# Optimization experiments

Hardware: AMD Instinct MI355X
Metric: run time of the kernel (lower is better)

Reference implementation:

```python
import jax, jax.numpy as jnp
import numpy as np

B, S, D = 512, 81, 1024
NH, DH = 16, 64
C, H1, G, FF = 32, 256, 256, 4096


def _ln(x, g, b, eps=1e-5):
    m = x.mean(-1, keepdims=True)
    v = ((x - m) ** 2).mean(-1, keepdims=True)
    return (x - m) * jax.lax.rsqrt(v + eps) * g + b


def _mish(x):
    return x * jnp.tanh(jax.nn.softplus(x))


def setup_inputs() -> dict:
    key = jax.random.key(0)
    ks = iter(jax.random.split(key, 32))
    n = lambda shape, s=0.02: jax.random.normal(next(ks), shape, jnp.float32) * s
    return {
        "x": jax.random.normal(next(ks), (B, S, D), jnp.float32),
        "w_compress": n((D, C)), "b_compress": jnp.zeros((C,)),
        "w_d1": n((S * C, H1)), "b_d1": jnp.zeros((H1,)),
        "ln1s_g": jnp.ones((H1,)), "ln1s_b": jnp.zeros((H1,)),
        "w_d2": n((H1, NH * G)), "b_d2": jnp.zeros((NH * G,)),
        "ln2s_g": jnp.ones((NH * G,)), "ln2s_b": jnp.zeros((NH * G,)),
        "w_gg": n((G, S * S)), "b_gg": jnp.zeros((S * S,)),
        "wq": n((D, D)), "bq": jnp.zeros((D,)),
        "wk": n((D, D)), "bk": jnp.zeros((D,)),
        "wv": n((D, D)), "bv": jnp.zeros((D,)),
        "wo": n((D, D)), "bo": jnp.zeros((D,)),
        "ln1_g": jnp.ones((D,)), "ln1_b": jnp.zeros((D,)),
        "w_f1": n((D, FF)), "b_f1": jnp.zeros((FF,)),
        "w_f2": n((FF, D)), "b_f2": jnp.zeros((D,)),
        "fln_g": jnp.ones((D,)), "fln_b": jnp.zeros((D,)),
    }


def reference(x, w_compress, b_compress, w_d1, b_d1, ln1s_g, ln1s_b,
              w_d2, b_d2, ln2s_g, ln2s_b, w_gg, b_gg,
              wq, bq, wk, bk, wv, bv, wo, bo, ln1_g, ln1_b,
              w_f1, b_f1, w_f2, b_f2, fln_g, fln_b):
    b = x.shape[0]
    # --- Smolgen: per-position attention bias ---
    h = jax.nn.silu(x @ w_compress + b_compress).reshape(b, S * C)
    h = jax.nn.silu(_ln(h @ w_d1 + b_d1, ln1s_g, ln1s_b))
    h = jax.nn.silu(_ln(h @ w_d2 + b_d2, ln2s_g, ln2s_b))
    h = h.reshape(b, NH, G)
    smol_bias = (h @ w_gg + b_gg).reshape(b, NH, S, S)
    # --- Attention with additive bias ---
    q = (x @ wq + bq).reshape(b, S, NH, DH)
    k = (x @ wk + bk).reshape(b, S, NH, DH)
    v = (x @ wv + bv).reshape(b, S, NH, DH)
    scores = jnp.einsum("bqhd,bkhd->bhqk", q, k) / np.sqrt(DH) + smol_bias
    attn = jax.nn.softmax(scores, axis=-1)
    out = jnp.einsum("bhqk,bkhd->bqhd", attn, v).reshape(b, S, D)
    h = _ln(out @ wo + bo + x, ln1_g, ln1_b)
    # --- FFN ---
    f = _mish(h @ w_f1 + b_f1)
    return _ln(f @ w_f2 + b_f2 + h, fln_g, fln_b)
```

## Files before the change

### kernel.cpp

```cpp
#include <hip/hip_runtime.h>
#include <hip/hip_bf16.h>
#include <cstdint>
#include <cstdio>

using bf16 = __hip_bfloat16;
typedef __attribute__((ext_vector_type(8))) short bf16x8;
typedef __attribute__((ext_vector_type(4))) float f32x4;

__device__ __forceinline__ void gload_lds16(const void* g, void* l) {
  __builtin_amdgcn_global_load_lds((__attribute__((address_space(1))) void*)g,
                                   (__attribute__((address_space(3))) void*)l,
                                   16, 0, 0);
}

__device__ __forceinline__ float bfu2f(unsigned short u) {
  return __uint_as_float((unsigned int)u << 16);
}
__device__ __forceinline__ unsigned short f2bfu(float f) {
  bf16 b = __float2bfloat16(f);
  return *(unsigned short*)&b;
}

enum { EP_NONE = 0, EP_SILU = 1, EP_MISH = 2, EP_RES = 3, EP_RESB = 4 };

template<int EPI>
__global__ __launch_bounds__(512, 1)
void gemm256(const bf16* __restrict__ A, const bf16* __restrict__ Bt,
             int N, int Nb, int K, int gx,
             const float* __restrict__ bias,
             const float* __restrict__ residf,
             const bf16* __restrict__ residb,
             bf16* __restrict__ outb)
{
  __shared__ char lds[131072];
  const int tid  = threadIdx.x;
  const int lane = tid & 63;
  const int wid  = tid >> 6;
  const int wm = wid >> 2, wn = wid & 3;
  const int lr = lane & 15, kg = lane >> 4;

  const int nwg = gridDim.x;
  const int q8 = nwg >> 3, r8 = nwg & 7;
  const int xcd = blockIdx.x & 7, idx = blockIdx.x >> 3;
  const int wg2 = (xcd < r8 ? xcd * (q8 + 1) : r8 * (q8 + 1) + (xcd - r8) * q8) + idx;
  const int bx = wg2 % gx, by = wg2 / gx;
  const long brow = (long)bx * 256, bcol = (long)by * 256;

  const size_t rb = (size_t)K * 2;
  const int r0   = wid * 8 + (lane >> 3);
  const int coff = ((lane & 7) ^ (lane >> 3)) << 4;
  const char* aS = (const char*)A  + (size_t)(brow + r0) * rb + coff;
  const char* bS = (const char*)Bt + (size_t)(bcol + r0) * rb + coff;
  char* ldsA = lds;
  char* ldsB = lds + 65536;
  const int luni = wid * 1024;

  const int ktiles = K >> 6;

  auto stage = [&](int t, int cur) {
    const size_t tb = (size_t)t * 128;
#pragma unroll
    for (int q = 0; q < 4; q++) {
      gload_lds16(aS + tb + (size_t)q * 64 * rb, ldsA + cur * 32768 + q * 8192 + luni);
      gload_lds16(bS + tb + (size_t)q * 64 * rb, ldsB + cur * 32768 + q * 8192 + luni);
    }
  };

  f32x4 acc[8][4] = {};

  stage(0, 0);
  stage(1, 1);

  const int swz   = (lr & 7) << 4;
  const int abase = (wm * 128 + lr) * 128;
  const int bbase = (wn * 64 + lr) * 128;

  for (int t = 0; t < ktiles; ++t) {
    const int cur = t & 1;
    if (t + 1 < ktiles) asm volatile("s_waitcnt vmcnt(8)" ::: "memory");
    else                asm volatile("s_waitcnt vmcnt(0)" ::: "memory");
    __builtin_amdgcn_s_barrier();
    const char* pA = ldsA + cur * 32768;
    const char* pB = ldsB + cur * 32768;
#pragma unroll
    for (int ks = 0; ks < 2; ks++) {
      const int kb = ((((ks << 2) + kg) << 4)) ^ swz;
      bf16x8 a[8], b[4];
#pragma unroll
      for (int i = 0; i < 8; i++) a[i] = *(const bf16x8*)(pA + abase + i * 2048 + kb);
#pragma unroll
      for (int j = 0; j < 4; j++) b[j] = *(const bf16x8*)(pB + bbase + j * 2048 + kb);
      __builtin_amdgcn_s_setprio(1);
#pragma unroll
      for (int i = 0; i < 8; i++)
#pragma unroll
        for (int j = 0; j < 4; j++)
          acc[i][j] = __builtin_amdgcn_mfma_f32_16x16x32_bf16(a[i], b[j], acc[i][j], 0, 0, 0);
      __builtin_amdgcn_s_setprio(0);
    }
    __builtin_amdgcn_s_barrier();
    if (t + 2 < ktiles) stage(t + 2, cur);
  }

  char* lC = lds;
  const int cr = kg * 4;
#pragma unroll
  for (int j = 0; j < 4; j++) {
    const int tcol = wn * 64 + j * 16 + lr;
    const long gcol = bcol + tcol;
    const float bv = (gcol < Nb) ? bias[gcol] : 0.f;
#pragma unroll
    for (int i = 0; i < 8; i++) {
#pragma unroll
      for (int r = 0; r < 4; r++) {
        const int row = wm * 128 + i * 16 + cr + r;
        float v = acc[i][j][r] + bv;
        if constexpr (EPI == EP_MISH) {
          float e = __expf(fminf(v, 20.f));
          float u = (1.f + e); u *= u;
          v = v * (u - 1.f) / (u + 1.f);
        }
        *(unsigned short*)(lC + row * 512 + ((tcol * 2) ^ ((row & 12) << 3))) = f2bfu(v);
      }
    }
  }
  __syncthreads();
  const int trow = tid >> 5;
  const int tcb  = (tid & 31) * 16;
#pragma unroll
  for (int it = 0; it < 16; ++it) {
    const int row = it * 16 + trow;
    bf16x8 vv = *(const bf16x8*)(lC + row * 512 + (tcb ^ ((row & 12) << 3)));
    const long grow = brow + row;
    bf16* dst = outb + grow * (long)N + bcol + (tcb >> 1);
    if constexpr (EPI == EP_RES) {
      const float* rs = residf + grow * (long)N + bcol + (tcb >> 1);
      float4 ra = *(const float4*)rs, rb2 = *(const float4*)(rs + 4);
      float rv[8] = {ra.x, ra.y, ra.z, ra.w, rb2.x, rb2.y, rb2.z, rb2.w};
      bf16x8 ov;
#pragma unroll
      for (int e = 0; e < 8; e++)
        ov[e] = (short)f2bfu(bfu2f((unsigned short)vv[e]) + rv[e]);
      *(bf16x8*)dst = ov;
    } else if constexpr (EPI == EP_RESB) {
      bf16x8 rb3 = *(const bf16x8*)(residb + grow * (long)N + bcol + (tcb >> 1));
      bf16x8 ov;
#pragma unroll
      for (int e = 0; e < 8; e++)
        ov[e] = (short)f2bfu(bfu2f((unsigned short)vv[e]) + bfu2f((unsigned short)rb3[e]));
      *(bf16x8*)dst = ov;
    } else {
      *(bf16x8*)dst = vv;
    }
  }
}

template<int EPI, bool OUTF>
__global__ __launch_bounds__(256)
void gemm_kernel(const bf16* __restrict__ A, const bf16* __restrict__ Bt,
                 int M, int N, int K,
                 const float* __restrict__ bias,
                 const float* __restrict__ residf,
                 const bf16* __restrict__ residb,
                 float* __restrict__ outf, bf16* __restrict__ outb)
{
  __shared__ bf16 lA[128 * 32];
  __shared__ bf16 lB[128 * 32];
  const int tid  = threadIdx.x;
  const int lane = tid & 63;
  const int wvid = tid >> 6;
  const int wr = (wvid >> 1) * 64;
  const int wc = (wvid & 1) * 64;
  const long brow = (long)blockIdx.x * 128;
  const long bcol = (long)blockIdx.y * 128;
  const int lr = lane & 15;
  const int k8 = (lane >> 4) * 8;

  const int lofs0 = wvid * 1024;
  const int lofs1 = lofs0 + 4096;
  const int o0 = lofs0 + lane * 16;
  const int o1 = o0 + 4096;
  const int r0 = o0 >> 6, c0 = o0 & 63;
  const int r1 = o1 >> 6, c1 = o1 & 63;

  f32x4 acc[4][4] = {};

  for (int k0 = 0; k0 < K; k0 += 32) {
    const long kb = (long)k0 * 2;
    gload_lds16((const char*)A  + ((brow + r0) * (long)K) * 2 + kb + c0, (char*)lA + lofs0);
    gload_lds16((const char*)A  + ((brow + r1) * (long)K) * 2 + kb + c1, (char*)lA + lofs1);
    gload_lds16((const char*)Bt + ((bcol + r0) * (long)K) * 2 + kb + c0, (char*)lB + lofs0);
    gload_lds16((const char*)Bt + ((bcol + r1) * (long)K) * 2 + kb + c1, (char*)lB + lofs1);
    __syncthreads();
    bf16x8 af[4], bf_[4];
#pragma unroll
    for (int i = 0; i < 4; i++)
      af[i] = *(const bf16x8*)&lA[(wr + i * 16 + lr) * 32 + k8];
#pragma unroll
    for (int j = 0; j < 4; j++)
      bf_[j] = *(const bf16x8*)&lB[(wc + j * 16 + lr) * 32 + k8];
#pragma unroll
    for (int i = 0; i < 4; i++)
#pragma unroll
      for (int j = 0; j < 4; j++)
        acc[i][j] = __builtin_amdgcn_mfma_f32_16x16x32_bf16(af[i], bf_[j], acc[i][j], 0, 0, 0);
    __syncthreads();
  }

  const int cr = (lane >> 4) * 4;
  const int cc = lane & 15;
#pragma unroll
  for (int j = 0; j < 4; j++) {
    const long col = bcol + wc + j * 16 + cc;
    if (col >= N) continue;
    const float bv = bias[col];
#pragma unroll
    for (int i = 0; i < 4; i++) {
#pragma unroll
      for (int r = 0; r < 4; r++) {
        const long row = brow + wr + i * 16 + cr + r;
        float v = acc[i][j][r] + bv;
        if constexpr (EPI == EP_RES)  v += residf[row * N + col];
        if constexpr (EPI == EP_RESB) v += __bfloat162float(residb[row * N + col]);
        if constexpr (EPI == EP_SILU) v = v / (1.f + __expf(-v));
        if constexpr (EPI == EP_MISH) {
          float t = __expf(fminf(v, 20.f));
          float u = (1.f + t); u *= u;
          v = v * (u - 1.f) / (u + 1.f);
        }
        if constexpr (OUTF) outf[row * N + col] = v;
        else                outb[row * N + col] = __float2bfloat16(v);
      }
    }
  }
}

__global__ __launch_bounds__(256)
void transpose_to_bf16(const float* __restrict__ W, bf16* __restrict__ Bt,
                       int K, int N, int Npad)
{
  __shared__ float tile[32][33];
  const int n0 = blockIdx.x * 32, k0 = blockIdx.y * 32;
  const int tx = threadIdx.x, ty = threadIdx.y;
  for (int r = ty; r < 32; r += 8) {
    int k = k0 + r, n = n0 + tx;
    tile[r][tx] = (k < K && n < N) ? W[(size_t)k * N + n] : 0.f;
  }
  __syncthreads();
  for (int r = ty; r < 32; r += 8) {
    int n = n0 + r, k = k0 + tx;
    if (n < Npad && k < K) Bt[(size_t)n * K + k] = __float2bfloat16(tile[tx][r]);
  }
}

__global__ __launch_bounds__(256)
void cvt_f32_bf16(const float* __restrict__ in, bf16* __restrict__ out, long n)
{
  long i = ((long)blockIdx.x * 256 + threadIdx.x) * 4;
  const long stride = (long)gridDim.x * 256 * 4;
  for (; i < n; i += stride) {
    float4 v = *(const float4*)(in + i);
    out[i]     = __float2bfloat16(v.x);
    out[i + 1] = __float2bfloat16(v.y);
    out[i + 2] = __float2bfloat16(v.z);
    out[i + 3] = __float2bfloat16(v.w);
  }
}

__global__ __launch_bounds__(256)
void pack3(const float* __restrict__ a, const float* __restrict__ b,
           const float* __restrict__ c, float* __restrict__ o, int n)
{
  int i = blockIdx.x * 256 + threadIdx.x;
  if (i < n) { o[i] = a[i]; o[n + i] = b[i]; o[2 * n + i] = c[i]; }
}

template<int ACT>
__global__ __launch_bounds__(256)
void ln_rows(const float* __restrict__ inf, const float* __restrict__ g,
             const float* __restrict__ be, bf16* __restrict__ ob, int C)
{
  const long row = blockIdx.x;
  float s = 0.f, ss = 0.f;
  for (int c = threadIdx.x; c < C; c += 256) {
    float v = inf[row * C + c];
    s += v; ss += v * v;
  }
#pragma unroll
  for (int o = 32; o; o >>= 1) { s += __shfl_xor(s, o); ss += __shfl_xor(ss, o); }
  __shared__ float p1[4], p2[4];
  const int wv = threadIdx.x >> 6;
  if ((threadIdx.x & 63) == 0) { p1[wv] = s; p2[wv] = ss; }
  __syncthreads();
  s  = p1[0] + p1[1] + p1[2] + p1[3];
  ss = p2[0] + p2[1] + p2[2] + p2[3];
  const float mean = s / C;
  const float var  = ss / C - mean * mean;
  const float rstd = rsqrtf(var + 1e-5f);
  for (int c = threadIdx.x; c < C; c += 256) {
    float v = (inf[row * C + c] - mean) * rstd * g[c] + be[c];
    if (ACT == 1) v = v / (1.f + __expf(-v));
    ob[row * C + c] = __float2bfloat16(v);
  }
}

template<bool WF, bool WB>
__global__ __launch_bounds__(256)
void ln1024(const bf16* __restrict__ inb, const float* __restrict__ g,
            const float* __restrict__ be, float* __restrict__ of,
            bf16* __restrict__ ob)
{
  const size_t row = blockIdx.x;
  const int t = threadIdx.x;
  const unsigned short* xr = (const unsigned short*)(inb + row * 1024) + t * 4;
  ushort4 raw = *(const ushort4*)xr;
  float v0 = bfu2f(raw.x), v1 = bfu2f(raw.y), v2 = bfu2f(raw.z), v3 = bfu2f(raw.w);
  float s = v0 + v1 + v2 + v3;
  float ss = v0 * v0 + v1 * v1 + v2 * v2 + v3 * v3;
#pragma unroll
  for (int o = 32; o; o >>= 1) { s += __shfl_xor(s, o); ss += __shfl_xor(ss, o); }
  __shared__ float p1[4], p2[4];
  const int wv = t >> 6;
  if ((t & 63) == 0) { p1[wv] = s; p2[wv] = ss; }
  __syncthreads();
  s  = p1[0] + p1[1] + p1[2] + p1[3];
  ss = p2[0] + p2[1] + p2[2] + p2[3];
  const float mean = s * (1.f / 1024.f);
  const float var  = ss * (1.f / 1024.f) - mean * mean;
  const float rstd = rsqrtf(var + 1e-5f);
  const int c = t * 4;
  float4 gg = *(const float4*)(g + c);
  float4 bb = *(const float4*)(be + c);
  float y0 = (v0 - mean) * rstd * gg.x + bb.x;
  float y1 = (v1 - mean) * rstd * gg.y + bb.y;
  float y2 = (v2 - mean) * rstd * gg.z + bb.z;
  float y3 = (v3 - mean) * rstd * gg.w + bb.w;
  if (WF) *(float4*)(of + row * 1024 + c) = make_float4(y0, y1, y2, y3);
  if (WB) {
    ushort4 o4 = { f2bfu(y0), f2bfu(y1), f2bfu(y2), f2bfu(y3) };
    *(ushort4*)((unsigned short*)(ob + row * 1024) + t * 4) = o4;
  }
}

__global__ __launch_bounds__(384)
void attn_mfma(const bf16* __restrict__ qkv, const bf16* __restrict__ smol,
               bf16* __restrict__ out)
{
  __shared__ char smem[37888];
  char* lqc = smem;
  char* lkc = smem + 12288;
  short* lvt = (short*)(smem + 24576);
  char* lpc = smem;

  const int b = blockIdx.x, h = blockIdx.y;
  const int tid = threadIdx.x;
  const int lane = tid & 63;
  const int w = tid >> 6;
  const int lr = lane & 15;
  const int kg = lane >> 4;

  const size_t qkv_base = (size_t)(b * 81) * 3072 + h * 64;

  for (int idx = tid; idx < 1296; idx += 384) {
    int which = idx >= 648;
    int e = which ? idx - 648 : idx;
    int s = e >> 3, c = e & 7;
    bf16x8 v = *(const bf16x8*)(qkv + qkv_base + (size_t)s * 3072 + which * 1024 + c * 8);
    char* base = which ? lkc : lqc;
    *(bf16x8*)(base + s * 128 + ((c ^ (s & 7)) << 4)) = v;
  }
  for (int idx = tid; idx < 648; idx += 384) {
    int s = idx >> 3, c = idx & 7;
    bf16x8 v = *(const bf16x8*)(qkv + qkv_base + (size_t)s * 3072 + 2048 + c * 8);
#pragma unroll
    for (int j = 0; j < 8; j++) lvt[(c * 8 + j) * 104 + s] = v[j];
  }
  {
    bf16x8 z = {};
    for (int idx = tid; idx < 240; idx += 384) {
      int which = idx >= 120;
      int e = which ? idx - 120 : idx;
      int s = 81 + (e >> 3), c = e & 7;
      char* base = which ? lkc : lqc;
      *(bf16x8*)(base + s * 128 + ((c ^ (s & 7)) << 4)) = z;
    }
    for (int idx = tid; idx < 1472; idx += 384) {
      int d = idx / 23, s = 81 + idx % 23;
      lvt[d * 104 + s] = 0;
    }
  }
  __syncthreads();

  f32x4 sacc[6] = {};
  const int m = w * 16 + lr;
#pragma unroll
  for (int ks = 0; ks < 2; ks++) {
    bf16x8 af = *(const bf16x8*)(lqc + m * 128 + ((((ks << 2) + kg) ^ (m & 7)) << 4));
#pragma unroll
    for (int j = 0; j < 6; j++) {
      int n = j * 16 + lr;
      bf16x8 bf_ = *(const bf16x8*)(lkc + n * 128 + ((((ks << 2) + kg) ^ (n & 7)) << 4));
      sacc[j] = __builtin_amdgcn_mfma_f32_16x16x32_bf16(af, bf_, sacc[j], 0, 0, 0);
    }
  }

  const bf16* smrow = smol + (size_t)(b * 16 + h) * 6656;
  float p[6][4];
#pragma unroll
  for (int j = 0; j < 6; j++) {
    int col = j * 16 + lr;
#pragma unroll
    for (int r = 0; r < 4; r++) {
      int row = w * 16 + kg * 4 + r;
      float sv = sacc[j][r] * 0.125f;
      if (col < 81) {
        if (row < 81) sv += __bfloat162float(smrow[row * 81 + col]);
      } else sv = -3.0e38f;
      p[j][r] = sv;
    }
  }
#pragma unroll
  for (int r = 0; r < 4; r++) {
    float mx = p[0][r];
#pragma unroll
    for (int j = 1; j < 6; j++) mx = fmaxf(mx, p[j][r]);
    mx = fmaxf(mx, __shfl_xor(mx, 1)); mx = fmaxf(mx, __shfl_xor(mx, 2));
    mx = fmaxf(mx, __shfl_xor(mx, 4)); mx = fmaxf(mx, __shfl_xor(mx, 8));
    float sum = 0.f;
#pragma unroll
    for (int j = 0; j < 6; j++) { float e = __expf(p[j][r] - mx); p[j][r] = e; sum += e; }
    sum += __shfl_xor(sum, 1); sum += __shfl_xor(sum, 2);
    sum += __shfl_xor(sum, 4); sum += __shfl_xor(sum, 8);
    float inv = 1.f / sum;
#pragma unroll
    for (int j = 0; j < 6; j++) p[j][r] *= inv;
  }
  __syncthreads();

#pragma unroll
  for (int j = 0; j < 6; j++) {
    int col = j * 16 + lr;
#pragma unroll
    for (int r = 0; r < 4; r++) {
      int row = w * 16 + kg * 4 + r;
      *(unsigned short*)(lpc + row * 256 + ((((col >> 3) ^ (row & 7)) << 4)) + (col & 7) * 2)
          = f2bfu(p[j][r]);
    }
  }
  __syncthreads();

  f32x4 oacc[4] = {};
#pragma unroll
  for (int ks = 0; ks < 3; ks++) {
    bf16x8 pa = *(const bf16x8*)(lpc + m * 256 + ((((ks << 2) + kg) ^ (m & 7)) << 4));
#pragma unroll
    for (int j2 = 0; j2 < 4; j2++) {
      int n = j2 * 16 + lr;
      bf16x8 vb = *(const bf16x8*)((char*)lvt + n * 208 + ((ks << 2) + kg) * 16);
      oacc[j2] = __builtin_amdgcn_mfma_f32_16x16x32_bf16(pa, vb, oacc[j2], 0, 0, 0);
    }
  }
#pragma unroll
  for (int j2 = 0; j2 < 4; j2++) {
    int d = j2 * 16 + lr;
#pragma unroll
    for (int r = 0; r < 4; r++) {
      int row = w * 16 + kg * 4 + r;
      if (row < 81)
        out[(size_t)(b * 81 + row) * 1024 + h * 64 + d] = __float2bfloat16(oacc[j2][r]);
    }
  }
}

extern "C" void kernel_launch(void* const* d_in, const int* in_sizes, int n_in,
                              void* d_out, int out_size, void* d_ws, size_t ws_size,
                              hipStream_t stream)
{
  const float* x     = (const float*)d_in[0];
  const float* w_c   = (const float*)d_in[1];
  const float* b_c   = (const float*)d_in[2];
  const float* w_d1  = (const float*)d_in[3];
  const float* b_d1  = (const float*)d_in[4];
  const float* ln1sg = (const float*)d_in[5];
  const float* ln1sb = (const float*)d_in[6];
  const float* w_d2  = (const float*)d_in[7];
  const float* b_d2  = (const float*)d_in[8];
  const float* ln2sg = (const float*)d_in[9];
  const float* ln2sb = (const float*)d_in[10];
  const float* w_gg  = (const float*)d_in[11];
  const float* b_gg  = (const float*)d_in[12];
  const float* wq    = (const float*)d_in[13];
  const float* bq    = (const float*)d_in[14];
  const float* wk    = (const float*)d_in[15];
  const float* bk    = (const float*)d_in[16];
  const float* wvp   = (const float*)d_in[17];
  const float* bv    = (const float*)d_in[18];
  const float* wo    = (const float*)d_in[19];
  const float* bo    = (const float*)d_in[20];
  const float* ln1g  = (const float*)d_in[21];
  const float* ln1b  = (const float*)d_in[22];
  const float* w_f1  = (const float*)d_in[23];
  const float* b_f1  = (const float*)d_in[24];
  const float* w_f2  = (const float*)d_in[25];
  const float* b_f2  = (const float*)d_in[26];
  const float* flng  = (const float*)d_in[27];
  const float* flnb  = (const float*)d_in[28];
  float* out = (float*)d_out;

  char* ws = (char*)d_ws;
  size_t off = 0;
  auto alloc = [&](size_t bytes) -> char* {
    char* p = ws + off; off += (bytes + 255) & ~(size_t)255; return p;
  };
  bf16*  Bt_c  = (bf16*)alloc(262144);
  bf16*  Bt_d1 = (bf16*)alloc(1327104);
  bf16*  Bt_d2 = (bf16*)alloc(2097152);
  bf16*  Bt_gg = (bf16*)alloc(3407872);
  bf16*  Bt_qkv= (bf16*)alloc(6291456);
  bf16*  Bt_wo = (bf16*)alloc(2097152);
  bf16*  Bt_f1 = (bf16*)alloc(8388608);
  bf16*  Bt_f2 = (bf16*)alloc(8388608);
  float* bqkv  = (float*)alloc(12288);
  bf16*  h0b   = (bf16*)alloc(2654208);
  float* pre_s = (float*)alloc(8388608);
  bf16*  h1b   = (bf16*)alloc(262144);
  bf16*  h2b   = (bf16*)alloc(4194304);
  char*  S1    = alloc(84934656);
  char*  S2    = alloc(339738624);
  char*  S3    = alloc(109051904);

  bf16* xb     = (bf16*)S1;
  bf16* hmidb  = (bf16*)S1;
  bf16* qkvb   = (bf16*)S2;
  bf16* aob    = (bf16*)(S2 + 254803968);
  bf16* fb     = (bf16*)S2;
  bf16* smol   = (bf16*)S3;
  bf16* preln1 = (bf16*)S3;
  bf16* preln2 = (bf16*)S3;

  if (ws_size < off) { printf("WS too small: %zu < %zu\n", ws_size, off); return; }

  const dim3 tb(32, 8);
  transpose_to_bf16<<<dim3(4, 32),   tb, 0, stream>>>(w_c,  Bt_c,  1024, 32,   128);
  transpose_to_bf16<<<dim3(8, 81),   tb, 0, stream>>>(w_d1, Bt_d1, 2592, 256,  256);
  transpose_to_bf16<<<dim3(128, 8),  tb, 0, stream>>>(w_d2, Bt_d2, 256,  4096, 4096);
  transpose_to_bf16<<<dim3(208, 8),  tb, 0, stream>>>(w_gg, Bt_gg, 256,  6561, 6656);
  transpose_to_bf16<<<dim3(32, 32),  tb, 0, stream>>>(wq,   Bt_qkv,             1024, 1024, 1024);
  transpose_to_bf16<<<dim3(32, 32),  tb, 0, stream>>>(wk,   Bt_qkv + 1024*1024, 1024, 1024, 1024);
  transpose_to_bf16<<<dim3(32, 32),  tb, 0, stream>>>(wvp,  Bt_qkv + 2048*1024, 1024, 1024, 1024);
  transpose_to_bf16<<<dim3(32, 32),  tb, 0, stream>>>(wo,   Bt_wo, 1024, 1024, 1024);
  transpose_to_bf16<<<dim3(128, 32), tb, 0, stream>>>(w_f1, Bt_f1, 1024, 4096, 4096);
  transpose_to_bf16<<<dim3(32, 128), tb, 0, stream>>>(w_f2, Bt_f2, 4096, 1024, 1024);
  pack3<<<4, 256, 0, stream>>>(bq, bk, bv, bqkv, 1024);
  cvt_f32_bf16<<<2048, 256, 0, stream>>>(x, xb, 42467328L);

  gemm_kernel<EP_SILU, false><<<dim3(324, 1), 256, 0, stream>>>(
      xb, Bt_c, 41472, 32, 1024, b_c, nullptr, nullptr, nullptr, h0b);
  gemm_kernel<EP_NONE, true><<<dim3(4, 2), 256, 0, stream>>>(
      h0b, Bt_d1, 512, 256, 2592, b_d1, nullptr, nullptr, pre_s, nullptr);
  ln_rows<1><<<512, 256, 0, stream>>>(pre_s, ln1sg, ln1sb, h1b, 256);
  gemm_kernel<EP_NONE, true><<<dim3(4, 32), 256, 0, stream>>>(
      h1b, Bt_d2, 512, 4096, 256, b_d2, nullptr, nullptr, pre_s, nullptr);
  ln_rows<1><<<512, 256, 0, stream>>>(pre_s, ln2sg, ln2sb, h2b, 4096);
  gemm256<EP_NONE><<<32 * 26, 512, 0, stream>>>(
      h2b, Bt_gg, 6656, 6561, 256, 32, b_gg, nullptr, nullptr, smol);

  gemm256<EP_NONE><<<162 * 12, 512, 0, stream>>>(
      xb, Bt_qkv, 3072, 3072, 1024, 162, bqkv, nullptr, nullptr, qkvb);
  attn_mfma<<<dim3(512, 16), 384, 0, stream>>>(qkvb, smol, aob);
  gemm256<EP_RESB><<<162 * 4, 512, 0, stream>>>(
      aob, Bt_wo, 1024, 1024, 1024, 162, bo, nullptr, xb, preln1);
  ln1024<false, true><<<41472, 256, 0, stream>>>(preln1, ln1g, ln1b, nullptr, hmidb);

  gemm256<EP_MISH><<<162 * 16, 512, 0, stream>>>(
      hmidb, Bt_f1, 4096, 4096, 1024, 162, b_f1, nullptr, nullptr, fb);
  gemm256<EP_RESB><<<162 * 4, 512, 0, stream>>>(
      fb, Bt_f2, 1024, 1024, 4096, 162, b_f2, nullptr, hmidb, preln2);
  ln1024<true, false><<<41472, 256, 0, stream>>>(preln2, flng, flnb, out, nullptr);
}
```

Before: 1.896 ms.

## Interleave GEMM global-to-LDS staging with MFMA quarter-steps in main loop

```diff
diff --git a/kernel.cpp b/kernel.cpp
--- a/kernel.cpp
+++ b/kernel.cpp
@@ -57,49 +57,99 @@
 
   const int ktiles = K >> 6;
 
-  auto stage = [&](int t, int cur) {
-    const size_t tb = (size_t)t * 128;
-#pragma unroll
-    for (int q = 0; q < 4; q++) {
-      gload_lds16(aS + tb + (size_t)q * 64 * rb, ldsA + cur * 32768 + q * 8192 + luni);
-      gload_lds16(bS + tb + (size_t)q * 64 * rb, ldsB + cur * 32768 + q * 8192 + luni);
-    }
+  auto stageA = [&](int t, int q) {
+    gload_lds16(aS + (size_t)t * 128 + (size_t)q * 64 * rb,
+                ldsA + (t & 1) * 32768 + q * 8192 + luni);
   };
+  auto stageB = [&](int t, int q) {
+    gload_lds16(bS + (size_t)t * 128 + (size_t)q * 64 * rb,
+                ldsB + (t & 1) * 32768 + q * 8192 + luni);
+  };
 
   f32x4 acc[8][4] = {};
 
-  stage(0, 0);
-  stage(1, 1);
+  stageA(0, 0); stageA(0, 2); stageB(0, 0); stageB(0, 1);
+  stageB(0, 2); stageB(0, 3); stageA(0, 1); stageA(0, 3);
+  if (ktiles > 1) { stageA(1, 0); stageA(1, 2); stageB(1, 0); stageB(1, 1); }
 
   const int swz   = (lr & 7) << 4;
+  const int kb0   = (kg << 4) ^ swz;
+  const int kb1   = ((4 + kg) << 4) ^ swz;
   const int abase = (wm * 128 + lr) * 128;
   const int bbase = (wn * 64 + lr) * 128;
 
   for (int t = 0; t < ktiles; ++t) {
-    const int cur = t & 1;
-    if (t + 1 < ktiles) asm volatile("s_waitcnt vmcnt(8)" ::: "memory");
+    const char* pA = ldsA + (t & 1) * 32768;
+    const char* pB = ldsB + (t & 1) * 32768;
+    bf16x8 af[4], b0[4], b1[4];
+
+    if (t + 1 < ktiles) asm volatile("s_waitcnt vmcnt(4)" ::: "memory");
     else                asm volatile("s_waitcnt vmcnt(0)" ::: "memory");
     __builtin_amdgcn_s_barrier();
-    const char* pA = ldsA + cur * 32768;
-    const char* pB = ldsB + cur * 32768;
-#pragma unroll
-    for (int ks = 0; ks < 2; ks++) {
-      const int kb = ((((ks << 2) + kg) << 4)) ^ swz;
-      bf16x8 a[8], b[4];
-#pragma unroll
-      for (int i = 0; i < 8; i++) a[i] = *(const bf16x8*)(pA + abase + i * 2048 + kb);
-#pragma unroll
-      for (int j = 0; j < 4; j++) b[j] = *(const bf16x8*)(pB + bbase + j * 2048 + kb);
-      __builtin_amdgcn_s_setprio(1);
-#pragma unroll
-      for (int i = 0; i < 8; i++)
-#pragma unroll
-        for (int j = 0; j < 4; j++)
-          acc[i][j] = __builtin_amdgcn_mfma_f32_16x16x32_bf16(a[i], b[j], acc[i][j], 0, 0, 0);
-      __builtin_amdgcn_s_setprio(0);
-    }
-    __builtin_amdgcn_s_barrier();
-    if (t + 2 < ktiles) stage(t + 2, cur);
+    __builtin_amdgcn_sched_barrier(0);
+#pragma unroll
+    for (int i = 0; i < 4; i++) af[i] = *(const bf16x8*)(pA + abase + i * 2048 + kb0);
+#pragma unroll
+    for (int j = 0; j < 4; j++) b0[j] = *(const bf16x8*)(pB + bbase + j * 2048 + kb0);
+    if (t + 1 < ktiles) { stageB(t + 1, 2); stageB(t + 1, 3); }
+    __builtin_amdgcn_s_barrier();
+    asm volatile("s_waitcnt lgkmcnt(0)" ::: "memory");
+    __builtin_amdgcn_sched_barrier(0);
+    __builtin_amdgcn_s_setprio(1);
+#pragma unroll
+    for (int i = 0; i < 4; i++)
+#pragma unroll
+      for (int j = 0; j < 4; j++)
+        acc[i][j] = __builtin_amdgcn_mfma_f32_16x16x32_bf16(af[i], b0[j], acc[i][j], 0, 0, 0);
+    __builtin_amdgcn_s_setprio(0);
+    __builtin_amdgcn_s_barrier();
+
+#pragma unroll
+    for (int i = 0; i < 4; i++) af[i] = *(const bf16x8*)(pA + abase + i * 2048 + kb1);
+#pragma unroll
+    for (int j = 0; j < 4; j++) b1[j] = *(const bf16x8*)(pB + bbase + j * 2048 + kb1);
+    if (t + 1 < ktiles) { stageA(t + 1, 1); stageA(t + 1, 3); }
+    __builtin_amdgcn_s_barrier();
+    asm volatile("s_waitcnt lgkmcnt(0)" ::: "memory");
+    __builtin_amdgcn_sched_barrier(0);
+    __builtin_amdgcn_s_setprio(1);
+#pragma unroll
+    for (int i = 0; i < 4; i++)
+#pragma unroll
+      for (int j = 0; j < 4; j++)
+        acc[i][j] = __builtin_amdgcn_mfma_f32_16x16x32_bf16(af[i], b1[j], acc[i][j], 0, 0, 0);
+    __builtin_amdgcn_s_setprio(0);
+    __builtin_amdgcn_s_barrier();
+
+#pragma unroll
+    for (int i = 0; i < 4; i++) af[i] = *(const bf16x8*)(pA + abase + (i + 4) * 2048 + kb0);
+    if (t + 2 < ktiles) { stageA(t + 2, 0); stageA(t + 2, 2); }
+    __builtin_amdgcn_s_barrier();
+    asm volatile("s_waitcnt lgkmcnt(0)" ::: "memory");
+    __builtin_amdgcn_sched_barrier(0);
+    __builtin_amdgcn_s_setprio(1);
+#pragma unroll
+    for (int i = 0; i < 4; i++)
+#pragma unroll
+      for (int j = 0; j < 4; j++)
+        acc[i + 4][j] = __builtin_amdgcn_mfma_f32_16x16x32_bf16(af[i], b0[j], acc[i + 4][j], 0, 0, 0);
+    __builtin_amdgcn_s_setprio(0);
+    __builtin_amdgcn_s_barrier();
+
+#pragma unroll
+    for (int i = 0; i < 4; i++) af[i] = *(const bf16x8*)(pA + abase + (i + 4) * 2048 + kb1);
+    if (t + 2 < ktiles) { stageB(t + 2, 0); stageB(t + 2, 1); }
+    __builtin_amdgcn_s_barrier();
+    asm volatile("s_waitcnt lgkmcnt(0)" ::: "memory");
+    __builtin_amdgcn_sched_barrier(0);
+    __builtin_amdgcn_s_setprio(1);
+#pragma unroll
+    for (int i = 0; i < 4; i++)
+#pragma unroll
+      for (int j = 0; j < 4; j++)
+        acc[i + 4][j] = __builtin_amdgcn_mfma_f32_16x16x32_bf16(af[i], b1[j], acc[i + 4][j], 0, 0, 0);
+    __builtin_amdgcn_s_setprio(0);
+    __builtin_amdgcn_s_barrier();
   }
 
   char* lC = lds;
```

After: 1.761 ms. 1.08x faster.

## Shrink gemm256 tile to 256x128 with K=32 stages for higher occupancy

Applied to the files above, without the earlier changes.

```diff
diff --git a/kernel.cpp b/kernel.cpp
--- a/kernel.cpp
+++ b/kernel.cpp
@@ -24,134 +24,131 @@
 enum { EP_NONE = 0, EP_SILU = 1, EP_MISH = 2, EP_RES = 3, EP_RESB = 4 };
 
 template<int EPI>
-__global__ __launch_bounds__(512, 1)
+__global__ __launch_bounds__(512, 4)
 void gemm256(const bf16* __restrict__ A, const bf16* __restrict__ Bt,
-             int N, int Nb, int K, int gx,
+             int N, int Nb, int K, int gy,
              const float* __restrict__ bias,
              const float* __restrict__ residf,
              const bf16* __restrict__ residb,
              bf16* __restrict__ outb)
 {
-  __shared__ char lds[131072];
+  __shared__ char lds[49152];
   const int tid  = threadIdx.x;
   const int lane = tid & 63;
   const int wid  = tid >> 6;
-  const int wm = wid >> 2, wn = wid & 3;
+  const int wm = wid >> 1, wn = wid & 1;
   const int lr = lane & 15, kg = lane >> 4;
 
   const int nwg = gridDim.x;
   const int q8 = nwg >> 3, r8 = nwg & 7;
   const int xcd = blockIdx.x & 7, idx = blockIdx.x >> 3;
   const int wg2 = (xcd < r8 ? xcd * (q8 + 1) : r8 * (q8 + 1) + (xcd - r8) * q8) + idx;
-  const int bx = wg2 % gx, by = wg2 / gx;
-  const long brow = (long)bx * 256, bcol = (long)by * 256;
+  const int bx = wg2 / gy, by = wg2 % gy;
+  const long brow = (long)bx * 256, bcol = (long)by * 128;
 
   const size_t rb = (size_t)K * 2;
-  const int r0   = wid * 8 + (lane >> 3);
-  const int coff = ((lane & 7) ^ (lane >> 3)) << 4;
-  const char* aS = (const char*)A  + (size_t)(brow + r0) * rb + coff;
-  const char* bS = (const char*)Bt + (size_t)(bcol + r0) * rb + coff;
+  const int srow = tid >> 2;
+  const int schk = (tid & 3) * 16;
+  const char* aS = (const char*)A  + (size_t)(brow + srow) * rb + schk;
+  const char* bS = (const char*)Bt + (size_t)(bcol + srow) * rb + schk;
   char* ldsA = lds;
-  char* ldsB = lds + 65536;
+  char* ldsB = lds + 32768;
   const int luni = wid * 1024;
 
-  const int ktiles = K >> 6;
-
-  auto stage = [&](int t, int cur) {
-    const size_t tb = (size_t)t * 128;
-#pragma unroll
-    for (int q = 0; q < 4; q++) {
-      gload_lds16(aS + tb + (size_t)q * 64 * rb, ldsA + cur * 32768 + q * 8192 + luni);
-      gload_lds16(bS + tb + (size_t)q * 64 * rb, ldsB + cur * 32768 + q * 8192 + luni);
-    }
+  const int ktiles = K >> 5;
+
+  auto stage = [&](int t) {
+    const size_t tb = (size_t)t * 64;
+    gload_lds16(aS + tb,                 ldsA + (t & 1) * 16384 + luni);
+    gload_lds16(aS + tb + 128 * rb,      ldsA + (t & 1) * 16384 + 8192 + luni);
+    gload_lds16(bS + tb,                 ldsB + (t & 1) * 8192 + luni);
   };
 
-  f32x4 acc[8][4] = {};
-
-  stage(0, 0);
-  stage(1, 1);
-
-  const int swz   = (lr & 7) << 4;
-  const int abase = (wm * 128 + lr) * 128;
-  const int bbase = (wn * 64 + lr) * 128;
+  f32x4 acc[4][4] = {};
+
+  stage(0);
+  stage(1);
+
+  const int abase = (wm * 64 + lr) * 64 + kg * 16;
+  const int bbase = (wn * 64 + lr) * 64 + kg * 16;
 
   for (int t = 0; t < ktiles; ++t) {
-    const int cur = t & 1;
-    if (t + 1 < ktiles) asm volatile("s_waitcnt vmcnt(8)" ::: "memory");
+    if (t + 1 < ktiles) asm volatile("s_waitcnt vmcnt(3)" ::: "memory");
     else                asm volatile("s_waitcnt vmcnt(0)" ::: "memory");
     __builtin_amdgcn_s_barrier();
-    const char* pA = ldsA + cur * 32768;
-    const char* pB = ldsB + cur * 32768;
-#pragma unroll
-    for (int ks = 0; ks < 2; ks++) {
-      const int kb = ((((ks << 2) + kg) << 4)) ^ swz;
-      bf16x8 a[8], b[4];
-#pragma unroll
-      for (int i = 0; i < 8; i++) a[i] = *(const bf16x8*)(pA + abase + i * 2048 + kb);
-#pragma unroll
-      for (int j = 0; j < 4; j++) b[j] = *(const bf16x8*)(pB + bbase + j * 2048 + kb);
-      __builtin_amdgcn_s_setprio(1);
-#pragma unroll
-      for (int i = 0; i < 8; i++)
-#pragma unroll
-        for (int j = 0; j < 4; j++)
-          acc[i][j] = __builtin_amdgcn_mfma_f32_16x16x32_bf16(a[i], b[j], acc[i][j], 0, 0, 0);
-      __builtin_amdgcn_s_setprio(0);
-    }
+    const char* pA = ldsA + (t & 1) * 16384;
+    const char* pB = ldsB + (t & 1) * 8192;
+    bf16x8 af[4], bf_[4];
+#pragma unroll
+    for (int i = 0; i < 4; i++) af[i]  = *(const bf16x8*)(pA + abase + i * 1024);
+#pragma unroll
+    for (int j = 0; j < 4; j++) bf_[j] = *(const bf16x8*)(pB + bbase + j * 1024);
+    __builtin_amdgcn_s_setprio(1);
+#pragma unroll
+    for (int i = 0; i < 4; i++)
+#pragma unroll
+      for (int j = 0; j < 4; j++)
+        acc[i][j] = __builtin_amdgcn_mfma_f32_16x16x32_bf16(af[i], bf_[j], acc[i][j], 0, 0, 0);
+    __builtin_amdgcn_s_setprio(0);
     __builtin_amdgcn_s_barrier();
-    if (t + 2 < ktiles) stage(t + 2, cur);
+    if (t + 2 < ktiles) stage(t + 2);
   }
 
   char* lC = lds;
-  const int cr = kg * 4;
-#pragma unroll
-  for (int j = 0; j < 4; j++) {
-    const int tcol = wn * 64 + j * 16 + lr;
-    const long gcol = bcol + tcol;
-    const float bv = (gcol < Nb) ? bias[gcol] : 0.f;
-#pragma unroll
-    for (int i = 0; i < 8; i++) {
-#pragma unroll
-      for (int r = 0; r < 4; r++) {
-        const int row = wm * 128 + i * 16 + cr + r;
-        float v = acc[i][j][r] + bv;
-        if constexpr (EPI == EP_MISH) {
-          float e = __expf(fminf(v, 20.f));
-          float u = (1.f + e); u *= u;
-          v = v * (u - 1.f) / (u + 1.f);
+#pragma unroll
+  for (int p = 0; p < 2; ++p) {
+    if ((wm >> 1) == p) {
+#pragma unroll
+      for (int j = 0; j < 4; j++) {
+        const int tcol = wn * 64 + j * 16 + lr;
+        const long gcol = bcol + tcol;
+        const float bv = (gcol < Nb) ? bias[gcol] : 0.f;
+#pragma unroll
+        for (int i = 0; i < 4; i++) {
+#pragma unroll
+          for (int r = 0; r < 4; r++) {
+            const int lrow = (wm & 1) * 64 + i * 16 + kg * 4 + r;
+            float v = acc[i][j][r] + bv;
+            if constexpr (EPI == EP_MISH) {
+              float e = __expf(fminf(v, 20.f));
+              float u = (1.f + e); u *= u;
+              v = v * (u - 1.f) / (u + 1.f);
+            }
+            *(unsigned short*)(lC + lrow * 256 + ((tcol * 2) ^ ((lrow & 12) << 3))) = f2bfu(v);
+          }
         }
-        *(unsigned short*)(lC + row * 512 + ((tcol * 2) ^ ((row & 12) << 3))) = f2bfu(v);
       }
     }
-  }
-  __syncthreads();
-  const int trow = tid >> 5;
-  const int tcb  = (tid & 31) * 16;
-#pragma unroll
-  for (int it = 0; it < 16; ++it) {
-    const int row = it * 16 + trow;
-    bf16x8 vv = *(const bf16x8*)(lC + row * 512 + (tcb ^ ((row & 12) << 3)));
-    const long grow = brow + row;
-    bf16* dst = outb + grow * (long)N + bcol + (tcb >> 1);
-    if constexpr (EPI == EP_RES) {
-      const float* rs = residf + grow * (long)N + bcol + (tcb >> 1);
-      float4 ra = *(const float4*)rs, rb2 = *(const float4*)(rs + 4);
-      float rv[8] = {ra.x, ra.y, ra.z, ra.w, rb2.x, rb2.y, rb2.z, rb2.w};
-      bf16x8 ov;
-#pragma unroll
-      for (int e = 0; e < 8; e++)
-        ov[e] = (short)f2bfu(bfu2f((unsigned short)vv[e]) + rv[e]);
-      *(bf16x8*)dst = ov;
-    } else if constexpr (EPI == EP_RESB) {
-      bf16x8 rb3 = *(const bf16x8*)(residb + grow * (long)N + bcol + (tcb >> 1));
-      bf16x8 ov;
-#pragma unroll
-      for (int e = 0; e < 8; e++)
-        ov[e] = (short)f2bfu(bfu2f((unsigned short)vv[e]) + bfu2f((unsigned short)rb3[e]));
-      *(bf16x8*)dst = ov;
-    } else {
-      *(bf16x8*)dst = vv;
-    }
+    __syncthreads();
+    const int trow = tid >> 4;
+    const int tcb  = (tid & 15) * 16;
+#pragma unroll
+    for (int it = 0; it < 4; ++it) {
+      const int lrow = it * 32 + trow;
+      bf16x8 vv = *(const bf16x8*)(lC + lrow * 256 + (tcb ^ ((lrow & 12) << 3)));
+      const long grow = brow + p * 128 + lrow;
+      bf16* dst = outb + grow * (long)N + bcol + (tcb >> 1);
+      if constexpr (EPI == EP_RES) {
+        const float* rs = residf + grow * (long)N + bcol + (tcb >> 1);
+        float4 ra = *(const float4*)rs, rb2 = *(const float4*)(rs + 4);
+        float rv[8] = {ra.x, ra.y, ra.z, ra.w, rb2.x, rb2.y, rb2.z, rb2.w};
+        bf16x8 ov;
+#pragma unroll
+        for (int e = 0; e < 8; e++)
+          ov[e] = (short)f2bfu(bfu2f((unsigned short)vv[e]) + rv[e]);
+        *(bf16x8*)dst = ov;
+      } else if constexpr (EPI == EP_RESB) {
+        bf16x8 rb3 = *(const bf16x8*)(residb + grow * (long)N + bcol + (tcb >> 1));
+        bf16x8 ov;
+#pragma unroll
+        for (int e = 0; e < 8; e++)
+          ov[e] = (short)f2bfu(bfu2f((unsigned short)vv[e]) + bfu2f((unsigned short)rb3[e]));
+        *(bf16x8*)dst = ov;
+      } else {
+        *(bf16x8*)dst = vv;
+      }
+    }
+    __syncthreads();
   }
 }
 
@@ -562,19 +559,19 @@
   gemm_kernel<EP_NONE, true><<<dim3(4, 32), 256, 0, stream>>>(
       h1b, Bt_d2, 512, 4096, 256, b_d2, nullptr, nullptr, pre_s, nullptr);
   ln_rows<1><<<512, 256, 0, stream>>>(pre_s, ln2sg, ln2sb, h2b, 4096);
-  gemm256<EP_NONE><<<32 * 26, 512, 0, stream>>>(
-      h2b, Bt_gg, 6656, 6561, 256, 32, b_gg, nullptr, nullptr, smol);
-
-  gemm256<EP_NONE><<<162 * 12, 512, 0, stream>>>(
-      xb, Bt_qkv, 3072, 3072, 1024, 162, bqkv, nullptr, nullptr, qkvb);
+  gemm256<EP_NONE><<<32 * 52, 512, 0, stream>>>(
+      h2b, Bt_gg, 6656, 6561, 256, 52, b_gg, nullptr, nullptr, smol);
+
+  gemm256<EP_NONE><<<162 * 24, 512, 0, stream>>>(
+      xb, Bt_qkv, 3072, 3072, 1024, 24, bqkv, nullptr, nullptr, qkvb);
   attn_mfma<<<dim3(512, 16), 384, 0, stream>>>(qkvb, smol, aob);
-  gemm256<EP_RESB><<<162 * 4, 512, 0, stream>>>(
-      aob, Bt_wo, 1024, 1024, 1024, 162, bo, nullptr, xb, preln1);
+  gemm256<EP_RESB><<<162 * 8, 512, 0, stream>>>(
+      aob, Bt_wo, 1024, 1024, 1024, 8, bo, nullptr, xb, preln1);
   ln1024<false, true><<<41472, 256, 0, stream>>>(preln1, ln1g, ln1b, nullptr, hmidb);
 
-  gemm256<EP_MISH><<<162 * 16, 512, 0, stream>>>(
-      hmidb, Bt_f1, 4096, 4096, 1024, 162, b_f1, nullptr, nullptr, fb);
-  gemm256<EP_RESB><<<162 * 4, 512, 0, stream>>>(
-      fb, Bt_f2, 1024, 1024, 4096, 162, b_f2, nullptr, hmidb, preln2);
+  gemm256<EP_MISH><<<162 * 32, 512, 0, stream>>>(
+      hmidb, Bt_f1, 4096, 4096, 1024, 32, b_f1, nullptr, nullptr, fb);
+  gemm256<EP_RESB><<<162 * 8, 512, 0, stream>>>(
+      fb, Bt_f2, 1024, 1024, 4096, 8, b_f2, nullptr, hmidb, preln2);
   ln1024<true, false><<<41472, 256, 0, stream>>>(preln2, flng, flnb, out, nullptr);
 }
```

New measurement: 1.841 ms. -2.9%, faster.
